# Performance work log

Hardware: AMD Instinct MI355X
Metric: run time of the kernel (lower is better)

## Reference

```python
import jax, jax.numpy as jnp
import numpy as np

CONF_THRES = 0.25
IOU_THRES = 0.45
MAX_DET = 1000
MAX_WH = 4096.0  # class offset used by YOLOv5 for class-aware NMS
K = 1024         # fixed candidate count (static-shape stand-in for conf filtering)


def xywh2xyxy(b):
    cx, cy, w, h = b[..., 0], b[..., 1], b[..., 2], b[..., 3]
    return jnp.stack([cx - w / 2, cy - h / 2, cx + w / 2, cy + h / 2], axis=-1)


def pairwise_iou(boxes):
    # boxes: [K,4] xyxy -> [K,K] IoU
    x1, y1, x2, y2 = boxes[:, 0], boxes[:, 1], boxes[:, 2], boxes[:, 3]
    area = (x2 - x1) * (y2 - y1)
    ix1 = jnp.maximum(x1[:, None], x1[None, :])
    iy1 = jnp.maximum(y1[:, None], y1[None, :])
    ix2 = jnp.minimum(x2[:, None], x2[None, :])
    iy2 = jnp.minimum(y2[:, None], y2[None, :])
    inter = jnp.clip(ix2 - ix1, 0.0) * jnp.clip(iy2 - iy1, 0.0)
    return inter / (area[:, None] + area[None, :] - inter + 1e-9)


def nms_image(pred):
    # pred: [N, 5+nc] = xywh, obj, class scores
    boxes = xywh2xyxy(pred[:, :4])                 # [N,4]
    scores = pred[:, 5:] * pred[:, 4:5]            # conf = obj * cls
    conf = jnp.max(scores, axis=-1)                # [N]
    cls = jnp.argmax(scores, axis=-1)              # [N] int
    masked = jnp.where(conf > CONF_THRES, conf, -1.0)
    top_conf, idx = jax.lax.top_k(masked, K)       # sorted desc
    cand_boxes = boxes[idx]                        # [K,4]
    cand_cls = cls[idx]                            # [K]
    cand_valid = top_conf > 0.0                    # below-threshold slots are -1
    # class-aware NMS: offset boxes per class so different classes never overlap
    off_boxes = cand_boxes + (cand_cls.astype(pred.dtype) * MAX_WH)[:, None]
    iou = pairwise_iou(off_boxes)                  # [K,K]

    def step(suppressed, i):
        keep_i = jnp.logical_and(jnp.logical_not(suppressed[i]), cand_valid[i])
        suppressed = jnp.where(keep_i, jnp.logical_or(suppressed, iou[i] > IOU_THRES), suppressed)
        return suppressed, keep_i

    _, keep = jax.lax.scan(step, jnp.zeros((K,), dtype=bool), jnp.arange(K))
    sel_score = jnp.where(keep, top_conf, -1.0)
    fin_score, fin_idx = jax.lax.top_k(sel_score, MAX_DET)
    ok = fin_score > 0.0
    det = jnp.concatenate(
        [cand_boxes[fin_idx],
         top_conf[fin_idx][:, None],
         cand_cls[fin_idx].astype(pred.dtype)[:, None]],
        axis=-1,
    )  # [MAX_DET, 6] = x1,y1,x2,y2,conf,cls
    return jnp.where(ok[:, None], det, 0.0)


def setup_inputs() -> dict:
    key = jax.random.key(0)
    k1, k2, k3, k4 = jax.random.split(key, 4)
    B, N, NC = 16, 25200, 80
    cxcy = jax.random.uniform(k1, (B, N, 2), dtype=jnp.float32) * 640.0
    wh = jax.random.uniform(k2, (B, N, 2), dtype=jnp.float32) * 96.0 + 4.0
    obj = jax.random.uniform(k3, (B, N, 1), dtype=jnp.float32)
    cls = jax.random.uniform(k4, (B, N, NC), dtype=jnp.float32)
    pred = jnp.concatenate([cxcy, wh, obj, cls], axis=-1)
    return {"pred": pred}


def reference(pred):
    # [B, MAX_DET, 6] zero-padded detections per image
    return jax.vmap(nms_image)(pred)
```

## Files before the change

### kernel.cpp

```cpp
#include <hip/hip_runtime.h>
#include <stdint.h>

typedef unsigned int u32;
typedef unsigned long long u64;

#define BB 16
#define NN 25200
#define ROWLEN 85
#define KCAND 1024
#define MAXDET 1000
#define CONF_T 0.25f
#define IOU_T 0.45f
#define MAX_WH 4096.0f
#define KBASE 0xBE800000u
#define NBLK 394

__device__ __forceinline__ u32 f2key(float f) {
  u32 u = __float_as_uint(f);
  return (u & 0x80000000u) ? ~u : (u | 0x80000000u);
}
__device__ __forceinline__ float key2f(u32 k) {
  u32 u = (k & 0x80000000u) ? (k & 0x7FFFFFFFu) : ~k;
  return __uint_as_float(u);
}

__global__ __launch_bounds__(64) void k_score(const float* __restrict__ pred,
                                              u32* __restrict__ keys,
                                              int* __restrict__ clsArr,
                                              u32* __restrict__ gh) {
  __shared__ float sh[64 * ROWLEN];
  __shared__ u32 h[256];
  const int t = threadIdx.x;
  const int bi = blockIdx.x;
  const int img = blockIdx.y;
  const int r0 = bi * 64;
  const float4* src = (const float4*)(pred + ((size_t)img * NN + r0) * ROWLEN);
  float4* dst = (float4*)sh;
  h[t] = 0u; h[t + 64] = 0u; h[t + 128] = 0u; h[t + 192] = 0u;
  if (r0 + 64 <= NN) {
    #pragma unroll
    for (int i = 0; i < 21; ++i) dst[t + 64 * i] = src[t + 64 * i];
    if (t < 16) dst[t + 64 * 21] = src[t + 64 * 21];
  } else {
    const int nf4 = (NN - r0) * ROWLEN / 4;
    for (int i = t; i < nf4; i += 64) dst[i] = src[i];
  }
  __syncthreads();
  const int nrows = (r0 + 64 <= NN) ? 64 : (NN - r0);
  if (t < nrows) {
    const float* row = sh + t * ROWLEN;
    float obj = row[4];
    float v0 = -INFINITY, v1 = -INFINITY, v2 = -INFINITY, v3 = -INFINITY;
    int j0 = 0, j1 = 20, j2 = 40, j3 = 60;
    #pragma unroll
    for (int c = 0; c < 20; ++c) {
      float s0 = obj * row[5 + c];
      float s1 = obj * row[25 + c];
      float s2 = obj * row[45 + c];
      float s3 = obj * row[65 + c];
      if (s0 > v0) { v0 = s0; j0 = c; }
      if (s1 > v1) { v1 = s1; j1 = 20 + c; }
      if (s2 > v2) { v2 = s2; j2 = 40 + c; }
      if (s3 > v3) { v3 = s3; j3 = 60 + c; }
    }
    float v = v0; int j = j0;
    if (v1 > v) { v = v1; j = j1; }
    if (v2 > v) { v = v2; j = j2; }
    if (v3 > v) { v = v3; j = j3; }
    u32 key = 0u;
    if (v > CONF_T) {
      key = f2key(v) - KBASE;
      atomicAdd(&h[key >> 16], 1u);
    }
    size_t r = (size_t)img * NN + r0 + t;
    keys[r] = key;
    clsArr[r] = j;
  }
  __syncthreads();
  u32* outp = gh + ((size_t)img * NBLK + bi) * 256;
  outp[t] = h[t]; outp[t + 64] = h[t + 64];
  outp[t + 128] = h[t + 128]; outp[t + 192] = h[t + 192];
}

__device__ __forceinline__ void bt_apply(u64& e, u64 p, int m, int j, int k) {
  bool lower = ((m & j) == 0);
  bool dir = ((m & k) == 0);
  bool takeMax = (lower == dir);
  u64 mx = e > p ? e : p;
  u64 mn = e > p ? p : e;
  e = takeMax ? mx : mn;
}

__global__ __launch_bounds__(1024, 4) void k_select(const float* __restrict__ pred,
                                                    const u32* __restrict__ keys,
                                                    const int* __restrict__ clsArr,
                                                    const u32* __restrict__ gh,
                                                    float* __restrict__ candScore,
                                                    float* __restrict__ candBox,
                                                    int* __restrict__ candCls) {
  __shared__ u32 hist4[4][256];
  __shared__ u32 hist1[257];
  __shared__ u64 buf[2048];
  __shared__ u32 sh_sel, sh_rem, sh_cnt;
  const int b = blockIdx.x;
  const int tid = threadIdx.x;
  const int lane = tid & 63;
  const int wv = tid >> 6;
  const u32* kk = keys + (size_t)b * NN;

  u32 rr[25];
  #pragma unroll
  for (int it = 0; it < 25; ++it) {
    int n0 = tid + it * 1024;
    rr[it] = (n0 < NN) ? kk[n0] : 0u;
  }

  {
    const int bin = tid & 255;
    const int part = tid >> 8;
    u32 csum = 0;
    const u32* g = gh + ((size_t)b * NBLK) * 256 + bin;
    for (int s = part; s < NBLK; s += 4) csum += g[(size_t)s << 8];
    hist4[part][bin] = csum;
  }
  if (tid == 0) sh_cnt = 0;
  __syncthreads();

  u32 prefix = 0, himask = 0, remaining = KCAND;
  if (wv == 0) {
    const int j4 = lane << 2;
    u32 c0 = hist4[0][j4 + 0] + hist4[1][j4 + 0] + hist4[2][j4 + 0] + hist4[3][j4 + 0];
    u32 c1 = hist4[0][j4 + 1] + hist4[1][j4 + 1] + hist4[2][j4 + 1] + hist4[3][j4 + 1];
    u32 c2 = hist4[0][j4 + 2] + hist4[1][j4 + 2] + hist4[2][j4 + 2] + hist4[3][j4 + 2];
    u32 c3 = hist4[0][j4 + 3] + hist4[1][j4 + 3] + hist4[2][j4 + 3] + hist4[3][j4 + 3];
    u32 tl = c0 + c1 + c2 + c3;
    u32 incl = tl;
    #pragma unroll
    for (int off = 1; off <= 32; off <<= 1) {
      u32 o = __shfl_down(incl, off, 64);
      if (lane + off < 64) incl += o;
    }
    u32 S0 = incl;
    u32 S1 = S0 - c0;
    u32 S2 = S1 - c1;
    u32 S3 = S2 - c2;
    u32 S4 = S3 - c3;
    u32 rem = remaining;
    if (S0 >= rem && S1 < rem) { sh_sel = 4 * lane + 0; sh_rem = rem - S1; }
    if (S1 >= rem && S2 < rem) { sh_sel = 4 * lane + 1; sh_rem = rem - S2; }
    if (S2 >= rem && S3 < rem) { sh_sel = 4 * lane + 2; sh_rem = rem - S3; }
    if (S3 >= rem && S4 < rem) { sh_sel = 4 * lane + 3; sh_rem = rem - S4; }
  }
  __syncthreads();
  prefix = (sh_sel << 16);
  remaining = sh_rem;
  himask = 0xFF0000u;

  #pragma unroll
  for (int pass = 1; pass < 3; ++pass) {
    const int shift = 16 - 8 * pass;
    if (tid < 256) hist1[tid] = 0u;
    __syncthreads();
    #pragma unroll
    for (int it = 0; it < 25; ++it) {
      u32 r = rr[it];
      if (r != 0u && (r & himask) == prefix)
        atomicAdd(&hist1[(r >> shift) & 255], 1u);
    }
    __syncthreads();
    if (wv == 0) {
      const int j4 = lane << 2;
      u32 c0 = hist1[j4 + 0], c1 = hist1[j4 + 1], c2 = hist1[j4 + 2], c3 = hist1[j4 + 3];
      u32 tl = c0 + c1 + c2 + c3;
      u32 incl = tl;
      #pragma unroll
      for (int off = 1; off <= 32; off <<= 1) {
        u32 o = __shfl_down(incl, off, 64);
        if (lane + off < 64) incl += o;
      }
      u32 S0 = incl;
      u32 S1 = S0 - c0;
      u32 S2 = S1 - c1;
      u32 S3 = S2 - c2;
      u32 S4 = S3 - c3;
      u32 rem = remaining;
      if (S0 >= rem && S1 < rem) { sh_sel = 4 * lane + 0; sh_rem = rem - S1; }
      if (S1 >= rem && S2 < rem) { sh_sel = 4 * lane + 1; sh_rem = rem - S2; }
      if (S2 >= rem && S3 < rem) { sh_sel = 4 * lane + 2; sh_rem = rem - S3; }
      if (S3 >= rem && S4 < rem) { sh_sel = 4 * lane + 3; sh_rem = rem - S4; }
    }
    __syncthreads();
    prefix |= (sh_sel << shift);
    remaining = sh_rem;
    himask |= (0xFFu << shift);
    __syncthreads();
  }
  const u32 T = prefix;

  #pragma unroll
  for (int it = 0; it < 25; ++it) {
    int n0 = tid + it * 1024;
    u32 r = rr[it];
    bool match = (r >= T);
    u64 bal = __ballot(match);
    if (bal) {
      int leader = __ffsll((unsigned long long)bal) - 1;
      u32 base = 0;
      u32 cnt = (u32)__popcll(bal);
      if (lane == leader) base = atomicAdd(&sh_cnt, cnt);
      base = __shfl(base, leader, 64);
      if (match) {
        u32 pos = base + (u32)__popcll(bal & ((1ull << lane) - 1ull));
        if (pos < 2048) buf[pos] = ((u64)r << 32) | (u32)(~(u32)n0);
      }
    }
  }
  __syncthreads();
  u32 c = sh_cnt; if (c > 2048) c = 2048;
  for (int t = tid; t < 2048; t += 1024) if (t >= (int)c) buf[t] = 0;
  __syncthreads();

  u64 e0 = buf[tid];
  u64 e1 = buf[tid + 1024];
  #pragma unroll
  for (int k = 2; k <= 64; k <<= 1) {
    #pragma unroll
    for (int j = k >> 1; j > 0; j >>= 1) {
      u64 p0 = __shfl_xor(e0, j, 64);
      u64 p1 = __shfl_xor(e1, j, 64);
      bt_apply(e0, p0, tid, j, k);
      bt_apply(e1, p1, tid + 1024, j, k);
    }
  }
  for (int k = 128; k <= 2048; k <<= 1) {
    int jstart = k >> 1;
    if (k == 2048) {
      u64 mx = e0 > e1 ? e0 : e1;
      u64 mn = e0 > e1 ? e1 : e0;
      e0 = mx; e1 = mn;
      jstart = 512;
    }
    for (int j = jstart; j >= 64; j >>= 1) {
      buf[tid] = e0; buf[tid + 1024] = e1;
      __syncthreads();
      u64 p0 = buf[tid ^ j];
      u64 p1 = buf[(tid ^ j) + 1024];
      bt_apply(e0, p0, tid, j, k);
      bt_apply(e1, p1, tid + 1024, j, k);
      __syncthreads();
    }
    #pragma unroll
    for (int j = 32; j > 0; j >>= 1) {
      u64 p0 = __shfl_xor(e0, j, 64);
      u64 p1 = __shfl_xor(e1, j, 64);
      bt_apply(e0, p0, tid, j, k);
      bt_apply(e1, p1, tid + 1024, j, k);
    }
  }
  {
    u64 e = e0;
    u32 r = (u32)(e >> 32);
    u32 idx = ~(u32)e;
    if (idx >= NN) idx = 0;
    float sc = key2f(r + KBASE);
    size_t g = (size_t)b * KCAND + tid;
    candScore[g] = sc;
    const float* p = pred + ((size_t)b * NN + idx) * ROWLEN;
    float cx = p[0], cy = p[1], w = p[2], h = p[3];
    float4 bx;
    bx.x = cx - 0.5f * w;
    bx.y = cy - 0.5f * h;
    bx.z = cx + 0.5f * w;
    bx.w = cy + 0.5f * h;
    ((float4*)candBox)[g] = bx;
    candCls[g] = clsArr[(size_t)b * NN + idx];
  }
}

__global__ __launch_bounds__(64) void k_iou(const float* __restrict__ candBox,
                                            const int* __restrict__ candCls,
                                            u64* __restrict__ matT) {
  #pragma clang fp contract(off)
  __shared__ float4 sb[64];
  __shared__ float sa[64];
  const int rc = blockIdx.x;
  const int cc = blockIdx.y;
  const int b  = blockIdx.z;
  if (rc > cc) return;
  const int lane = threadIdx.x;
  {
    int rrow = rc * 64 + lane;
    float4 bx = ((const float4*)candBox)[(size_t)b * KCAND + rrow];
    float off = (float)candCls[(size_t)b * KCAND + rrow] * MAX_WH;
    float x1 = bx.x + off, y1 = bx.y + off, x2 = bx.z + off, y2 = bx.w + off;
    float4 sbv; sbv.x = x1; sbv.y = y1; sbv.z = x2; sbv.w = y2;
    sb[lane] = sbv;
    sa[lane] = (x2 - x1) * (y2 - y1);
  }
  int col = cc * 64 + lane;
  float4 cb = ((const float4*)candBox)[(size_t)b * KCAND + col];
  float coff = (float)candCls[(size_t)b * KCAND + col] * MAX_WH;
  float cx1 = cb.x + coff, cy1 = cb.y + coff, cx2 = cb.z + coff, cy2 = cb.w + coff;
  float car = (cx2 - cx1) * (cy2 - cy1);
  __syncthreads();
  u64 myw = 0;
  for (int r = 0; r < 64; ++r) {
    float4 rb = sb[r];
    float ra = sa[r];
    float ix1 = fmaxf(rb.x, cx1);
    float iy1 = fmaxf(rb.y, cy1);
    float ix2 = fminf(rb.z, cx2);
    float iy2 = fminf(rb.w, cy2);
    float dx = fmaxf(ix2 - ix1, 0.0f);
    float dy = fmaxf(iy2 - iy1, 0.0f);
    float inter = dx * dy;
    float den = ra + car;
    den = den - inter;
    den = den + 1e-9f;
    float iou = inter / den;
    u64 bal = __ballot(iou > IOU_T);
    if (lane == r) myw = bal;
  }
  matT[(((size_t)b * 16 + cc) << 10) + rc * 64 + lane] = myw;
}

#define TRIDX(c, cp) (((c) * ((c)-1)) / 2 + (cp))
__global__ __launch_bounds__(256, 1) void k_scan_out(const u64* __restrict__ matT,
                                                     const float* __restrict__ candScore,
                                                     const float* __restrict__ candBox,
                                                     const int* __restrict__ candCls,
                                                     float* __restrict__ out) {
  __shared__ u64 sKeep[16];
  const int b = blockIdx.x;
  const int tid = threadIdx.x;
  const u64* Mb = matT + ((size_t)b << 14);

  if (tid < 64) {
    const int lane = tid;
    u64 vw[16], dg[16], tri[120], kcw[16];
    #pragma unroll
    for (int w = 0; w < 16; ++w) {
      float sc = candScore[(size_t)b * KCAND + w * 64 + lane];
      vw[w] = __ballot(sc > 0.0f);
    }
    #pragma unroll
    for (int c = 0; c < 16; ++c)
      dg[c] = Mb[((size_t)c << 10) + c * 64 + lane];
    #pragma unroll
    for (int c = 1; c < 16; ++c) {
      #pragma unroll
      for (int cp = 0; cp < c; ++cp)
        tri[TRIDX(c, cp)] = Mb[((size_t)c << 10) + cp * 64 + lane];
    }

    #pragma unroll
    for (int c = 0; c < 16; ++c) {
      u64 acc = 0;
      #pragma unroll
      for (int cp = 0; cp < 15; ++cp) {
        if (cp < c) {
          if ((kcw[cp] >> lane) & 1ull) acc |= tri[TRIDX(c, cp)];
        }
      }
      #pragma unroll
      for (int st = 1; st < 64; st <<= 1) acc |= __shfl_xor(acc, st, 64);
      u64 d = dg[c];
      u64 s = acc;
      u64 kc = 0;
      u64 vc = vw[c];
      #pragma unroll
      for (int g = 0; g < 8; ++g) {
        u64 dgp[8];
        #pragma unroll
        for (int j = 0; j < 8; ++j) dgp[j] = __shfl(d, g * 8 + j, 64);
        #pragma unroll
        for (int j = 0; j < 8; ++j) {
          int i = g * 8 + j;
          bool ok = !((s >> i) & 1ull) && ((vc >> i) & 1ull);
          if (ok) { s |= dgp[j]; kc |= (1ull << i); }
        }
      }
      kcw[c] = kc;
    }
    if (lane < 16) sKeep[lane] = kcw[lane];
  }
  __syncthreads();

  int total = 0;
  #pragma unroll
  for (int w = 0; w < 16; ++w) total += __popcll(sKeep[w]);
  int kept_eff = total < MAXDET ? total : MAXDET;
  float* outb = out + (size_t)b * MAXDET * 6;
  #pragma unroll
  for (int rr2 = 0; rr2 < 4; ++rr2) {
    const int t = tid + rr2 * 256;
    u64 word = sKeep[t >> 6];
    int bit = (int)((word >> (t & 63)) & 1ull);
    int rank = 0;
    for (int w = 0; w < (t >> 6); ++w) rank += __popcll(sKeep[w]);
    rank += __popcll(word & ((1ull << (t & 63)) - 1ull));
    if (bit && rank < MAXDET) {
      size_t g = (size_t)b * KCAND + t;
      float4 bx = ((const float4*)candBox)[g];
      float sc = candScore[g];
      float cf = (float)candCls[g];
      float* o = outb + (size_t)rank * 6;
      o[0] = bx.x; o[1] = bx.y; o[2] = bx.z; o[3] = bx.w; o[4] = sc; o[5] = cf;
    }
    if (t < MAXDET && t >= kept_eff) {
      float* o = outb + (size_t)t * 6;
      o[0] = 0.f; o[1] = 0.f; o[2] = 0.f; o[3] = 0.f; o[4] = 0.f; o[5] = 0.f;
    }
  }
}

extern "C" void kernel_launch(void* const* d_in, const int* in_sizes, int n_in,
                              void* d_out, int out_size, void* d_ws, size_t ws_size,
                              hipStream_t stream) {
  const float* pred = (const float*)d_in[0];
  float* out = (float*)d_out;
  char* ws = (char*)d_ws;
  size_t o = 0;
  u32*   keysW     = (u32*)  (ws + o); o += (size_t)BB * NN * 4;
  int*   clsArr    = (int*)  (ws + o); o += (size_t)BB * NN * 4;
  u32*   gh        = (u32*)  (ws + o); o += (size_t)BB * NBLK * 256 * 4;
  float* candScore = (float*)(ws + o); o += (size_t)BB * KCAND * 4;
  float* candBox   = (float*)(ws + o); o += (size_t)BB * KCAND * 16;
  int*   candCls   = (int*)  (ws + o); o += (size_t)BB * KCAND * 4;
  o = (o + 255) & ~(size_t)255;
  u64*   matT      = (u64*)  (ws + o); o += (size_t)BB * KCAND * 16 * 8;

  k_score<<<dim3(NBLK, BB), 64, 0, stream>>>(pred, keysW, clsArr, gh);
  k_select<<<BB, 1024, 0, stream>>>(pred, keysW, clsArr, gh, candScore, candBox, candCls);
  k_iou<<<dim3(16, 16, BB), 64, 0, stream>>>(candBox, candCls, matT);
  k_scan_out<<<BB, 256, 0, stream>>>(matT, candScore, candBox, candCls, out);
}
```

Before: 317.0 us.

## Build top-level histogram inside select kernel and sort only 1024 when possible

Removes the per-block 256-bin histograms that the scoring kernel wrote to global memory, along with the select kernel's reduction over 394 partial histograms per image. The select kernel instead builds the top radix histogram from its register-resident keys, using per-wave shared-memory sub-histograms. It also adds a path that runs a single-element 1024-wide bitonic sort when at most 1024 candidates match, avoiding the 2048-wide sort. The trade-off is more shared-memory atomic work in a kernel that runs only one block per image, and an extra branch.

```diff
diff --git a/kernel.cpp b/kernel.cpp
--- a/kernel.cpp
+++ b/kernel.cpp
@@ -26,17 +26,14 @@
 
 __global__ __launch_bounds__(64) void k_score(const float* __restrict__ pred,
                                               u32* __restrict__ keys,
-                                              int* __restrict__ clsArr,
-                                              u32* __restrict__ gh) {
+                                              int* __restrict__ clsArr) {
   __shared__ float sh[64 * ROWLEN];
-  __shared__ u32 h[256];
   const int t = threadIdx.x;
   const int bi = blockIdx.x;
   const int img = blockIdx.y;
   const int r0 = bi * 64;
   const float4* src = (const float4*)(pred + ((size_t)img * NN + r0) * ROWLEN);
   float4* dst = (float4*)sh;
-  h[t] = 0u; h[t + 64] = 0u; h[t + 128] = 0u; h[t + 192] = 0u;
   if (r0 + 64 <= NN) {
     #pragma unroll
     for (int i = 0; i < 21; ++i) dst[t + 64 * i] = src[t + 64 * i];
@@ -67,19 +64,11 @@
     if (v1 > v) { v = v1; j = j1; }
     if (v2 > v) { v = v2; j = j2; }
     if (v3 > v) { v = v3; j = j3; }
-    u32 key = 0u;
-    if (v > CONF_T) {
-      key = f2key(v) - KBASE;
-      atomicAdd(&h[key >> 16], 1u);
-    }
+    u32 key = (v > CONF_T) ? (f2key(v) - KBASE) : 0u;
     size_t r = (size_t)img * NN + r0 + t;
     keys[r] = key;
     clsArr[r] = j;
   }
-  __syncthreads();
-  u32* outp = gh + ((size_t)img * NBLK + bi) * 256;
-  outp[t] = h[t]; outp[t + 64] = h[t + 64];
-  outp[t + 128] = h[t + 128]; outp[t + 192] = h[t + 192];
 }
 
 __device__ __forceinline__ void bt_apply(u64& e, u64 p, int m, int j, int k) {
@@ -94,11 +83,10 @@
 __global__ __launch_bounds__(1024, 4) void k_select(const float* __restrict__ pred,
                                                     const u32* __restrict__ keys,
                                                     const int* __restrict__ clsArr,
-                                                    const u32* __restrict__ gh,
                                                     float* __restrict__ candScore,
                                                     float* __restrict__ candBox,
                                                     int* __restrict__ candCls) {
-  __shared__ u32 hist4[4][256];
+  __shared__ u32 hist[16][257];
   __shared__ u32 hist1[257];
   __shared__ u64 buf[2048];
   __shared__ u32 sh_sel, sh_rem, sh_cnt;
@@ -107,6 +95,7 @@
   const int lane = tid & 63;
   const int wv = tid >> 6;
   const u32* kk = keys + (size_t)b * NN;
+  u32* histflat = (u32*)hist;
 
   u32 rr[25];
   #pragma unroll
@@ -115,24 +104,24 @@
     rr[it] = (n0 < NN) ? kk[n0] : 0u;
   }
 
-  {
-    const int bin = tid & 255;
-    const int part = tid >> 8;
-    u32 csum = 0;
-    const u32* g = gh + ((size_t)b * NBLK) * 256 + bin;
-    for (int s = part; s < NBLK; s += 4) csum += g[(size_t)s << 8];
-    hist4[part][bin] = csum;
-  }
+  for (int i = tid; i < 16 * 257; i += 1024) histflat[i] = 0;
   if (tid == 0) sh_cnt = 0;
   __syncthreads();
-
-  u32 prefix = 0, himask = 0, remaining = KCAND;
+  #pragma unroll
+  for (int it = 0; it < 25; ++it) {
+    u32 r = rr[it];
+    if (r != 0u) atomicAdd(&hist[wv][r >> 16], 1u);
+  }
+  __syncthreads();
   if (wv == 0) {
-    const int j4 = lane << 2;
-    u32 c0 = hist4[0][j4 + 0] + hist4[1][j4 + 0] + hist4[2][j4 + 0] + hist4[3][j4 + 0];
-    u32 c1 = hist4[0][j4 + 1] + hist4[1][j4 + 1] + hist4[2][j4 + 1] + hist4[3][j4 + 1];
-    u32 c2 = hist4[0][j4 + 2] + hist4[1][j4 + 2] + hist4[2][j4 + 2] + hist4[3][j4 + 2];
-    u32 c3 = hist4[0][j4 + 3] + hist4[1][j4 + 3] + hist4[2][j4 + 3] + hist4[3][j4 + 3];
+    u32 c0 = 0, c1 = 0, c2 = 0, c3 = 0;
+    #pragma unroll
+    for (int w = 0; w < 16; ++w) {
+      c0 += hist[w][4 * lane + 0];
+      c1 += hist[w][4 * lane + 1];
+      c2 += hist[w][4 * lane + 2];
+      c3 += hist[w][4 * lane + 3];
+    }
     u32 tl = c0 + c1 + c2 + c3;
     u32 incl = tl;
     #pragma unroll
@@ -145,16 +134,17 @@
     u32 S2 = S1 - c1;
     u32 S3 = S2 - c2;
     u32 S4 = S3 - c3;
-    u32 rem = remaining;
+    u32 rem = KCAND;
     if (S0 >= rem && S1 < rem) { sh_sel = 4 * lane + 0; sh_rem = rem - S1; }
     if (S1 >= rem && S2 < rem) { sh_sel = 4 * lane + 1; sh_rem = rem - S2; }
     if (S2 >= rem && S3 < rem) { sh_sel = 4 * lane + 2; sh_rem = rem - S3; }
     if (S3 >= rem && S4 < rem) { sh_sel = 4 * lane + 3; sh_rem = rem - S4; }
   }
   __syncthreads();
-  prefix = (sh_sel << 16);
-  remaining = sh_rem;
-  himask = 0xFF0000u;
+  u32 prefix = (sh_sel << 16);
+  u32 remaining = sh_rem;
+  u32 himask = 0xFF0000u;
+  __syncthreads();
 
   #pragma unroll
   for (int pass = 1; pass < 3; ++pass) {
@@ -221,40 +211,65 @@
   __syncthreads();
 
   u64 e0 = buf[tid];
-  u64 e1 = buf[tid + 1024];
-  #pragma unroll
-  for (int k = 2; k <= 64; k <<= 1) {
-    #pragma unroll
-    for (int j = k >> 1; j > 0; j >>= 1) {
-      u64 p0 = __shfl_xor(e0, j, 64);
-      u64 p1 = __shfl_xor(e1, j, 64);
-      bt_apply(e0, p0, tid, j, k);
-      bt_apply(e1, p1, tid + 1024, j, k);
-    }
-  }
-  for (int k = 128; k <= 2048; k <<= 1) {
-    int jstart = k >> 1;
-    if (k == 2048) {
-      u64 mx = e0 > e1 ? e0 : e1;
-      u64 mn = e0 > e1 ? e1 : e0;
-      e0 = mx; e1 = mn;
-      jstart = 512;
-    }
-    for (int j = jstart; j >= 64; j >>= 1) {
-      buf[tid] = e0; buf[tid + 1024] = e1;
-      __syncthreads();
-      u64 p0 = buf[tid ^ j];
-      u64 p1 = buf[(tid ^ j) + 1024];
-      bt_apply(e0, p0, tid, j, k);
-      bt_apply(e1, p1, tid + 1024, j, k);
-      __syncthreads();
-    }
-    #pragma unroll
-    for (int j = 32; j > 0; j >>= 1) {
-      u64 p0 = __shfl_xor(e0, j, 64);
-      u64 p1 = __shfl_xor(e1, j, 64);
-      bt_apply(e0, p0, tid, j, k);
-      bt_apply(e1, p1, tid + 1024, j, k);
+  if (c <= 1024) {
+    #pragma unroll
+    for (int k = 2; k <= 64; k <<= 1) {
+      #pragma unroll
+      for (int j = k >> 1; j > 0; j >>= 1) {
+        u64 p0 = __shfl_xor(e0, j, 64);
+        bt_apply(e0, p0, tid, j, k);
+      }
+    }
+    for (int k = 128; k <= 1024; k <<= 1) {
+      for (int j = k >> 1; j >= 64; j >>= 1) {
+        buf[tid] = e0;
+        __syncthreads();
+        u64 p0 = buf[tid ^ j];
+        bt_apply(e0, p0, tid, j, k);
+        __syncthreads();
+      }
+      #pragma unroll
+      for (int j = 32; j > 0; j >>= 1) {
+        u64 p0 = __shfl_xor(e0, j, 64);
+        bt_apply(e0, p0, tid, j, k);
+      }
+    }
+  } else {
+    u64 e1 = buf[tid + 1024];
+    #pragma unroll
+    for (int k = 2; k <= 64; k <<= 1) {
+      #pragma unroll
+      for (int j = k >> 1; j > 0; j >>= 1) {
+        u64 p0 = __shfl_xor(e0, j, 64);
+        u64 p1 = __shfl_xor(e1, j, 64);
+        bt_apply(e0, p0, tid, j, k);
+        bt_apply(e1, p1, tid + 1024, j, k);
+      }
+    }
+    for (int k = 128; k <= 2048; k <<= 1) {
+      int jstart = k >> 1;
+      if (k == 2048) {
+        u64 mx = e0 > e1 ? e0 : e1;
+        u64 mn = e0 > e1 ? e1 : e0;
+        e0 = mx; e1 = mn;
+        jstart = 512;
+      }
+      for (int j = jstart; j >= 64; j >>= 1) {
+        buf[tid] = e0; buf[tid + 1024] = e1;
+        __syncthreads();
+        u64 p0 = buf[tid ^ j];
+        u64 p1 = buf[(tid ^ j) + 1024];
+        bt_apply(e0, p0, tid, j, k);
+        bt_apply(e1, p1, tid + 1024, j, k);
+        __syncthreads();
+      }
+      #pragma unroll
+      for (int j = 32; j > 0; j >>= 1) {
+        u64 p0 = __shfl_xor(e0, j, 64);
+        u64 p1 = __shfl_xor(e1, j, 64);
+        bt_apply(e0, p0, tid, j, k);
+        bt_apply(e1, p1, tid + 1024, j, k);
+      }
     }
   }
   {
@@ -423,15 +438,14 @@
   size_t o = 0;
   u32*   keysW     = (u32*)  (ws + o); o += (size_t)BB * NN * 4;
   int*   clsArr    = (int*)  (ws + o); o += (size_t)BB * NN * 4;
-  u32*   gh        = (u32*)  (ws + o); o += (size_t)BB * NBLK * 256 * 4;
   float* candScore = (float*)(ws + o); o += (size_t)BB * KCAND * 4;
   float* candBox   = (float*)(ws + o); o += (size_t)BB * KCAND * 16;
   int*   candCls   = (int*)  (ws + o); o += (size_t)BB * KCAND * 4;
   o = (o + 255) & ~(size_t)255;
   u64*   matT      = (u64*)  (ws + o); o += (size_t)BB * KCAND * 16 * 8;
 
-  k_score<<<dim3(NBLK, BB), 64, 0, stream>>>(pred, keysW, clsArr, gh);
-  k_select<<<BB, 1024, 0, stream>>>(pred, keysW, clsArr, gh, candScore, candBox, candCls);
+  k_score<<<dim3(NBLK, BB), 64, 0, stream>>>(pred, keysW, clsArr);
+  k_select<<<BB, 1024, 0, stream>>>(pred, keysW, clsArr, candScore, candBox, candCls);
   k_iou<<<dim3(16, 16, BB), 64, 0, stream>>>(candBox, candCls, matT);
   k_scan_out<<<BB, 256, 0, stream>>>(matT, candScore, candBox, candCls, out);
 }
```

Result: slower. 470.9 us (+48.6%).
